# Optimization experiments

Measured on AMD Instinct MI355X. Metric: run time of the kernel, lower is better.

Reference implementation:

```python
import jax, jax.numpy as jnp
import numpy as np
import math

H = 8          # num_heads
HD = 64        # head_dim = hidden_dim // num_heads
LN_EPS = 1e-5


def setup_inputs() -> dict:
    key = jax.random.key(0)
    ks = jax.random.split(key, 16)
    B, N, L, D = 16, 1024, 7, 512
    s = 1.0 / math.sqrt(D)
    current_features = jax.random.normal(ks[0], (B, N, D), jnp.float32)
    lagged_features = jax.random.normal(ks[1], (B, N, L, D), jnp.float32)
    lag_weights = jnp.ones((L,), jnp.float32)
    Wq = jax.random.normal(ks[2], (D, D), jnp.float32) * s
    bq = jnp.zeros((D,), jnp.float32)
    Wk = jax.random.normal(ks[3], (D, D), jnp.float32) * s
    bk = jnp.zeros((D,), jnp.float32)
    Wv = jax.random.normal(ks[4], (D, D), jnp.float32) * s
    bv = jnp.zeros((D,), jnp.float32)
    Wo = jax.random.normal(ks[5], (D, D), jnp.float32) * s
    bo = jnp.zeros((D,), jnp.float32)
    adj = jax.random.uniform(ks[6], (N, N), jnp.float32)
    adj_prior = adj / (jnp.sum(adj, axis=-1, keepdims=True) + 1e-8)
    ln_g = jnp.ones((D,), jnp.float32)
    ln_b = jnp.zeros((D,), jnp.float32)
    return dict(current_features=current_features, lagged_features=lagged_features,
                lag_weights=lag_weights, Wq=Wq, bq=bq, Wk=Wk, bk=bk, Wv=Wv, bv=bv,
                Wo=Wo, bo=bo, adj_prior=adj_prior, ln_g=ln_g, ln_b=ln_b)


def _layer_norm(x, g, b):
    mu = jnp.mean(x, axis=-1, keepdims=True)
    var = jnp.mean(jnp.square(x - mu), axis=-1, keepdims=True)
    return (x - mu) * jax.lax.rsqrt(var + LN_EPS) * g + b


def reference(current_features, lagged_features, lag_weights, Wq, bq, Wk, bk,
              Wv, bv, Wo, bo, adj_prior, ln_g, ln_b):
    B, N, D = current_features.shape
    # lag-weighted aggregation of past states
    lag_w = jax.nn.softmax(lag_weights)
    lagged_agg = jnp.einsum('bnld,l->bnd', lagged_features, lag_w)
    # projections (torch Linear: x @ W.T + b)
    Q = current_features @ Wq.T + bq
    K = lagged_agg @ Wk.T + bk
    V = lagged_agg @ Wv.T + bv
    Q = Q.reshape(B, N, H, HD)
    K = K.reshape(B, N, H, HD)
    V = V.reshape(B, N, H, HD)
    scale = math.sqrt(HD)
    # scores [B, H, N, N] with additive adjacency bias
    scores = jnp.einsum('bnhd,bmhd->bhnm', Q, K) / scale
    scores = scores + adj_prior[None, None, :, :] * 0.5
    attn = jax.nn.softmax(scores, axis=-1)
    out = jnp.einsum('bhnm,bmhd->bnhd', attn, V).reshape(B, N, D)
    out = out @ Wo.T + bo
    return _layer_norm(current_features + out, ln_g, ln_b)
```

## Files before the change

kernel.cpp:

```cpp
#include <hip/hip_runtime.h>
#include <math.h>

#define B_  16
#define N_  1024
#define L_  7
#define D_  512
#define H_  8
#define HD_ 64
#define BN_ (B_ * N_)

typedef __attribute__((ext_vector_type(4))) float f32x4;
typedef __attribute__((ext_vector_type(8))) short bf16x8;

__device__ __forceinline__ unsigned short f2bf(float f) {
  unsigned int u = __float_as_uint(f);
  u += 0x7fffu + ((u >> 16) & 1u);
  return (unsigned short)(u >> 16);
}
__device__ __forceinline__ unsigned int pack2(float lo, float hi) {
  return (unsigned int)f2bf(lo) | ((unsigned int)f2bf(hi) << 16);
}
__device__ __forceinline__ void load_lds16(const unsigned short* g, unsigned short* s) {
  __builtin_amdgcn_global_load_lds(
      (const __attribute__((address_space(1))) void*)g,
      (__attribute__((address_space(3))) void*)s, 16, 0, 0);
}

__global__ __launch_bounds__(256)
void cast_bf16_kernel(const float* __restrict__ src, unsigned short* __restrict__ dst,
                      int n8) {
  const int i = blockIdx.x * 256 + threadIdx.x;
  if (i >= n8) return;
  const float4 a = ((const float4*)src)[2 * i];
  const float4 b = ((const float4*)src)[2 * i + 1];
  uint4 o;
  o.x = pack2(a.x, a.y); o.y = pack2(a.z, a.w);
  o.z = pack2(b.x, b.y); o.w = pack2(b.z, b.w);
  ((uint4*)dst)[i] = o;
}

__global__ __launch_bounds__(256)
void cast_w4_kernel(const float* __restrict__ w0, const float* __restrict__ w1,
                    const float* __restrict__ w2, const float* __restrict__ w3,
                    unsigned short* __restrict__ o0, unsigned short* __restrict__ o1,
                    unsigned short* __restrict__ o2, unsigned short* __restrict__ o3) {
  const int y = blockIdx.y;
  const float* src = (y == 0) ? w0 : (y == 1) ? w1 : (y == 2) ? w2 : w3;
  unsigned short* dst = (y == 0) ? o0 : (y == 1) ? o1 : (y == 2) ? o2 : o3;
  const int i = blockIdx.x * 256 + threadIdx.x;
  const float4 a = ((const float4*)src)[2 * i];
  const float4 b = ((const float4*)src)[2 * i + 1];
  uint4 o;
  o.x = pack2(a.x, a.y); o.y = pack2(a.z, a.w);
  o.z = pack2(b.x, b.y); o.w = pack2(b.z, b.w);
  ((uint4*)dst)[i] = o;
}

__global__ __launch_bounds__(256)
void lag_agg_bf16_kernel(const float* __restrict__ lf, const float* __restrict__ lw,
                         unsigned short* __restrict__ out) {
  const int i = blockIdx.x * 256 + threadIdx.x;
  float wv[L_];
  float m = -INFINITY;
#pragma unroll
  for (int l = 0; l < L_; ++l) { wv[l] = lw[l]; m = fmaxf(m, wv[l]); }
  float s = 0.f;
#pragma unroll
  for (int l = 0; l < L_; ++l) { wv[l] = __expf(wv[l] - m); s += wv[l]; }
  const float inv = 1.f / s;

  const int d8 = i & (D_ / 8 - 1);
  const int bn = i >> 6;
  const float* src = lf + (size_t)bn * (L_ * D_) + d8 * 8;
  float acc[8] = {};
#pragma unroll
  for (int l = 0; l < L_; ++l) {
    const float4 v0 = *(const float4*)(src + l * D_);
    const float4 v1 = *(const float4*)(src + l * D_ + 4);
    const float wl = wv[l] * inv;
    acc[0] += v0.x * wl; acc[1] += v0.y * wl; acc[2] += v0.z * wl; acc[3] += v0.w * wl;
    acc[4] += v1.x * wl; acc[5] += v1.y * wl; acc[6] += v1.z * wl; acc[7] += v1.w * wl;
  }
  uint4 o;
  o.x = pack2(acc[0], acc[1]); o.y = pack2(acc[2], acc[3]);
  o.z = pack2(acc[4], acc[5]); o.w = pack2(acc[6], acc[7]);
  ((uint4*)out)[i] = o;
}

struct GJob {
  const unsigned short* A;
  const unsigned short* W;
  const float* bias;
  void* C;
  int mode;
};

__global__ __launch_bounds__(256)
void gemm_dbuf_kernel(GJob j0, GJob j1, GJob j2) {
  const GJob j = (blockIdx.z == 0) ? j0 : (blockIdx.z == 1) ? j1 : j2;
  __shared__ unsigned short As[2 * 128 * 64];
  __shared__ unsigned short Bs[2 * 128 * 64];
  const int t = threadIdx.x;
  const int w = t >> 6, l = t & 63;
  const int wm = w >> 1, wn = w & 1;
  const int lc = l & 15, lg = l >> 4;
  const int m0 = blockIdx.y << 7, n0 = blockIdx.x << 7;
  const int srow = l >> 3, sc = l & 7;
  const unsigned short* A = j.A;
  const unsigned short* W = j.W;

  f32x4 acc[4][4];
#pragma unroll
  for (int i = 0; i < 4; ++i)
#pragma unroll
    for (int jj = 0; jj < 4; ++jj)
#pragma unroll
      for (int e = 0; e < 4; ++e) acc[i][jj][e] = 0.f;

#pragma unroll
  for (int i = 0; i < 4; ++i) {
    const int rb = (w << 5) + (i << 3);
    const int row = rb + srow;
    const int c = sc ^ (row & 7);
    load_lds16(A + (size_t)(m0 + row) * D_ + (c << 3), As + rb * 64);
    load_lds16(W + (size_t)(n0 + row) * D_ + (c << 3), Bs + rb * 64);
  }

  int cur = 0;
  for (int k0 = 0; k0 < D_; k0 += 64) {
    __syncthreads();
    if (k0 + 64 < D_) {
      unsigned short* An = As + ((cur ^ 1) << 13);
      unsigned short* Bn = Bs + ((cur ^ 1) << 13);
#pragma unroll
      for (int i = 0; i < 4; ++i) {
        const int rb = (w << 5) + (i << 3);
        const int row = rb + srow;
        const int c = sc ^ (row & 7);
        load_lds16(A + (size_t)(m0 + row) * D_ + k0 + 64 + (c << 3), An + rb * 64);
        load_lds16(W + (size_t)(n0 + row) * D_ + k0 + 64 + (c << 3), Bn + rb * 64);
      }
    }
    const unsigned short* Ac = As + (cur << 13);
    const unsigned short* Bc = Bs + (cur << 13);
#pragma unroll
    for (int kb = 0; kb < 2; ++kb) {
      bf16x8 af[4], bfr[4];
#pragma unroll
      for (int mi = 0; mi < 4; ++mi) {
        const int row = (wm << 6) + (mi << 4) + lc;
        const int pos = ((kb << 2) + lg) ^ (row & 7);
        af[mi] = *(const bf16x8*)(Ac + row * 64 + (pos << 3));
      }
#pragma unroll
      for (int ni = 0; ni < 4; ++ni) {
        const int row = (wn << 6) + (ni << 4) + lc;
        const int pos = ((kb << 2) + lg) ^ (row & 7);
        bfr[ni] = *(const bf16x8*)(Bc + row * 64 + (pos << 3));
      }
#pragma unroll
      for (int mi = 0; mi < 4; ++mi)
#pragma unroll
        for (int ni = 0; ni < 4; ++ni)
          acc[mi][ni] = __builtin_amdgcn_mfma_f32_16x16x32_bf16(
              af[mi], bfr[ni], acc[mi][ni], 0, 0, 0);
    }
    cur ^= 1;
  }

  const int mode = j.mode;
#pragma unroll
  for (int ni = 0; ni < 4; ++ni) {
    const int n = n0 + (wn << 6) + (ni << 4) + lc;
    const float bv = j.bias[n];
#pragma unroll
    for (int mi = 0; mi < 4; ++mi) {
      const int mb = m0 + (wm << 6) + (mi << 4) + (lg << 2);
      if (mode == 2) {
        float* O = (float*)j.C;
#pragma unroll
        for (int e = 0; e < 4; ++e)
          O[(size_t)(mb + e) * D_ + n] = acc[mi][ni][e] + bv;
      } else if (mode == 0) {
        unsigned short* O = (unsigned short*)j.C;
#pragma unroll
        for (int e = 0; e < 4; ++e)
          O[(size_t)(mb + e) * D_ + n] = f2bf(acc[mi][ni][e] + bv);
      } else {
        unsigned short* O = (unsigned short*)j.C;
        const int bb = mb >> 10, hh = n >> 6, d = n & 63;
        uint2 pk;
        pk.x = pack2(acc[mi][ni][0] + bv, acc[mi][ni][1] + bv);
        pk.y = pack2(acc[mi][ni][2] + bv, acc[mi][ni][3] + bv);
        *(uint2*)(O + ((size_t)((bb << 3) + hh) * HD_ + d) * N_ + (mb & 1023)) = pk;
      }
    }
  }
}

__global__ __launch_bounds__(256)
void attn_bf16_kernel(const unsigned short* __restrict__ Q,
                      const unsigned short* __restrict__ K,
                      const unsigned short* __restrict__ Vt,
                      const float* __restrict__ adj,
                      unsigned short* __restrict__ Out) {
  const int bh = blockIdx.y, b = bh >> 3, h = bh & 7;
  const int q0 = blockIdx.x << 6;
  const int t = threadIdx.x, w = t >> 6, l = t & 63;
  const int lc = l & 15, lg = l >> 4;
  __shared__ unsigned short Qs[64 * 64];
  __shared__ unsigned short Ks[2 * 64 * 64];
  __shared__ unsigned short Vs[2 * 64 * 64];
  const unsigned short* Qg = Q + (size_t)b * N_ * D_ + h * HD_;
  const unsigned short* Kg = K + (size_t)b * N_ * D_ + h * HD_;
  const unsigned short* Vg = Vt + (size_t)((b << 3) + h) * HD_ * N_;

#pragma unroll
  for (int i = 0; i < 2; ++i) {
    const int rb = (w << 4) + (i << 3);
    const int row = rb + (l >> 3);
    const int c = (l & 7) ^ (row & 7);
    load_lds16(Qg + (size_t)(q0 + row) * D_ + (c << 3), Qs + rb * 64);
    load_lds16(Kg + (size_t)row * D_ + (c << 3), Ks + rb * 64);
    load_lds16(Vg + (size_t)row * N_ + (c << 3), Vs + rb * 64);
  }
  __syncthreads();

  bf16x8 qf[2];
#pragma unroll
  for (int kb = 0; kb < 2; ++kb) {
    const int row = (w << 4) + lc;
    const int pos = ((kb << 2) + lg) ^ (row & 7);
    qf[kb] = *(const bf16x8*)(Qs + row * 64 + (pos << 3));
  }

  float m_r = -INFINITY, l_r = 0.f;
  f32x4 o[4];
#pragma unroll
  for (int di = 0; di < 4; ++di)
#pragma unroll
    for (int e = 0; e < 4; ++e) o[di][e] = 0.f;
  const int myq = q0 + (w << 4) + lc;
  unsigned short* Pw = Qs + (w << 10);

  int cur = 0;
  for (int kt = 0; kt < 16; ++kt) {
    if (kt) __syncthreads();
    const int kv0 = kt << 6;
    if (kt < 15) {
      unsigned short* Kn = Ks + ((cur ^ 1) << 12);
      unsigned short* Vn = Vs + ((cur ^ 1) << 12);
#pragma unroll
      for (int i = 0; i < 2; ++i) {
        const int rb = (w << 4) + (i << 3);
        const int row = rb + (l >> 3);
        const int c = (l & 7) ^ (row & 7);
        load_lds16(Kg + (size_t)(kv0 + 64 + row) * D_ + (c << 3), Kn + rb * 64);
        load_lds16(Vg + (size_t)row * N_ + kv0 + 64 + (c << 3), Vn + rb * 64);
      }
    }
    f32x4 aj[4];
#pragma unroll
    for (int ni = 0; ni < 4; ++ni)
      aj[ni] = *(const f32x4*)(adj + (size_t)myq * N_ + kv0 + (ni << 4) + (lg << 2));

    const unsigned short* Kc = Ks + (cur << 12);
    const unsigned short* Vc = Vs + (cur << 12);

    f32x4 st[4];
#pragma unroll
    for (int ni = 0; ni < 4; ++ni)
#pragma unroll
      for (int e = 0; e < 4; ++e) st[ni][e] = 0.f;
#pragma unroll
    for (int ni = 0; ni < 4; ++ni)
#pragma unroll
      for (int kb = 0; kb < 2; ++kb) {
        const int row = (ni << 4) + lc;
        const int pos = ((kb << 2) + lg) ^ (row & 7);
        const bf16x8 kf = *(const bf16x8*)(Kc + row * 64 + (pos << 3));
        st[ni] = __builtin_amdgcn_mfma_f32_16x16x32_bf16(kf, qf[kb], st[ni], 0, 0, 0);
      }

    float tmax = -INFINITY;
#pragma unroll
    for (int ni = 0; ni < 4; ++ni)
#pragma unroll
      for (int e = 0; e < 4; ++e) {
        const float v = st[ni][e] * 0.125f + 0.5f * aj[ni][e];
        st[ni][e] = v;
        tmax = fmaxf(tmax, v);
      }
    tmax = fmaxf(tmax, __shfl_xor(tmax, 16));
    tmax = fmaxf(tmax, __shfl_xor(tmax, 32));
    const float mnew = fmaxf(m_r, tmax);
    const float alpha = __expf(m_r - mnew);
    float ts = 0.f;
#pragma unroll
    for (int ni = 0; ni < 4; ++ni)
#pragma unroll
      for (int e = 0; e < 4; ++e) {
        const float p = __expf(st[ni][e] - mnew);
        st[ni][e] = p;
        ts += p;
      }
    ts += __shfl_xor(ts, 16);
    ts += __shfl_xor(ts, 32);
    l_r = l_r * alpha + ts;
    m_r = mnew;
#pragma unroll
    for (int di = 0; di < 4; ++di)
#pragma unroll
      for (int e = 0; e < 4; ++e) o[di][e] *= alpha;

#pragma unroll
    for (int ni = 0; ni < 4; ++ni) {
      uint2 pr;
      pr.x = pack2(st[ni][0], st[ni][1]);
      pr.y = pack2(st[ni][2], st[ni][3]);
      const int schunk = (2 * ni + (lg >> 1)) ^ (lc & 7);
      *(uint2*)(Pw + lc * 64 + (schunk << 3) + ((lg & 1) << 2)) = pr;
    }

#pragma unroll
    for (int kb = 0; kb < 2; ++kb) {
      const int rchunk = ((kb << 2) + lg) ^ (lc & 7);
      const bf16x8 pb = *(const bf16x8*)(Pw + lc * 64 + (rchunk << 3));
#pragma unroll
      for (int di = 0; di < 4; ++di) {
        const int row = (di << 4) + lc;
        const int pos = ((kb << 2) + lg) ^ (row & 7);
        const bf16x8 vf = *(const bf16x8*)(Vc + row * 64 + (pos << 3));
        o[di] = __builtin_amdgcn_mfma_f32_16x16x32_bf16(vf, pb, o[di], 0, 0, 0);
      }
    }
    cur ^= 1;
  }

  const float inv = 1.f / l_r;
  unsigned short* Ob = Out + (size_t)(b * N_ + q0 + (w << 4) + lc) * D_ + h * HD_;
#pragma unroll
  for (int di = 0; di < 4; ++di) {
    uint2 pk;
    pk.x = pack2(o[di][0] * inv, o[di][1] * inv);
    pk.y = pack2(o[di][2] * inv, o[di][3] * inv);
    *(uint2*)(Ob + (di << 4) + (lg << 2)) = pk;
  }
}

__global__ __launch_bounds__(256)
void ln_kernel(float* __restrict__ Y, const float* __restrict__ Xr,
               const float* __restrict__ g, const float* __restrict__ bta) {
  const int row  = (blockIdx.x << 2) + (threadIdx.x >> 6);
  const int lane = threadIdx.x & 63;
  float* yrow = Y + (size_t)row * D_;
  const float* xrow = Xr + (size_t)row * D_;
  const int c0 = lane << 3;

  const float4 y0 = *(const float4*)(yrow + c0);
  const float4 y1 = *(const float4*)(yrow + c0 + 4);
  const float4 r0 = *(const float4*)(xrow + c0);
  const float4 r1 = *(const float4*)(xrow + c0 + 4);
  float x[8] = {y0.x + r0.x, y0.y + r0.y, y0.z + r0.z, y0.w + r0.w,
                y1.x + r1.x, y1.y + r1.y, y1.z + r1.z, y1.w + r1.w};

  float sum = 0.f;
#pragma unroll
  for (int u = 0; u < 8; ++u) sum += x[u];
#pragma unroll
  for (int off = 32; off >= 1; off >>= 1) sum += __shfl_xor(sum, off);
  const float mu = sum * (1.f / D_);

  float vs = 0.f;
#pragma unroll
  for (int u = 0; u < 8; ++u) { const float d = x[u] - mu; vs += d * d; }
#pragma unroll
  for (int off = 32; off >= 1; off >>= 1) vs += __shfl_xor(vs, off);
  const float var = vs * (1.f / D_) + 1e-5f;
  float rinv = rsqrtf(var);
  rinv = rinv * (1.5f - 0.5f * var * rinv * rinv);

  const float4 g0 = *(const float4*)(g + c0);
  const float4 g1 = *(const float4*)(g + c0 + 4);
  const float4 b0 = *(const float4*)(bta + c0);
  const float4 b1 = *(const float4*)(bta + c0 + 4);
  float4 o0, o1;
  o0.x = (x[0] - mu) * rinv * g0.x + b0.x;
  o0.y = (x[1] - mu) * rinv * g0.y + b0.y;
  o0.z = (x[2] - mu) * rinv * g0.z + b0.z;
  o0.w = (x[3] - mu) * rinv * g0.w + b0.w;
  o1.x = (x[4] - mu) * rinv * g1.x + b1.x;
  o1.y = (x[5] - mu) * rinv * g1.y + b1.y;
  o1.z = (x[6] - mu) * rinv * g1.z + b1.z;
  o1.w = (x[7] - mu) * rinv * g1.w + b1.w;
  *(float4*)(yrow + c0) = o0;
  *(float4*)(yrow + c0 + 4) = o1;
}

extern "C" void kernel_launch(void* const* d_in, const int* in_sizes, int n_in,
                              void* d_out, int out_size, void* d_ws, size_t ws_size,
                              hipStream_t stream) {
  const float* cur = (const float*)d_in[0];
  const float* lf  = (const float*)d_in[1];
  const float* lw  = (const float*)d_in[2];
  const float* Wq  = (const float*)d_in[3];
  const float* bq  = (const float*)d_in[4];
  const float* Wk  = (const float*)d_in[5];
  const float* bk  = (const float*)d_in[6];
  const float* Wv  = (const float*)d_in[7];
  const float* bv  = (const float*)d_in[8];
  const float* Wo  = (const float*)d_in[9];
  const float* bo  = (const float*)d_in[10];
  const float* adj = (const float*)d_in[11];
  const float* lng = (const float*)d_in[12];
  const float* lnb = (const float*)d_in[13];
  float* out = (float*)d_out;

  const size_t NE = (size_t)BN_ * D_;
  unsigned short* wsb   = (unsigned short*)d_ws;
  unsigned short* curb  = wsb;
  unsigned short* laggb = wsb + NE;
  unsigned short* Qb    = wsb + 2 * NE;
  unsigned short* Kb    = wsb + 3 * NE;
  unsigned short* Vtb   = wsb + 4 * NE;
  unsigned short* attnb = wsb + 5 * NE;
  unsigned short* Wqb   = wsb + 6 * NE;
  unsigned short* Wkb   = Wqb + (size_t)D_ * D_;
  unsigned short* Wvb   = Wkb + (size_t)D_ * D_;
  unsigned short* Wob   = Wvb + (size_t)D_ * D_;

  cast_bf16_kernel<<<BN_ * D_ / 8 / 256, 256, 0, stream>>>(cur, curb, BN_ * D_ / 8);
  cast_w4_kernel<<<dim3(D_ * D_ / 8 / 256, 4), 256, 0, stream>>>(
      Wq, Wk, Wv, Wo, Wqb, Wkb, Wvb, Wob);
  lag_agg_bf16_kernel<<<BN_ * D_ / 8 / 256, 256, 0, stream>>>(lf, lw, laggb);

  GJob jq{curb,  Wqb, bq, (void*)Qb,  0};
  GJob jk{laggb, Wkb, bk, (void*)Kb,  0};
  GJob jv{laggb, Wvb, bv, (void*)Vtb, 1};
  gemm_dbuf_kernel<<<dim3(D_ / 128, BN_ / 128, 3), 256, 0, stream>>>(jq, jk, jv);

  attn_bf16_kernel<<<dim3(N_ / 64, B_ * H_), 256, 0, stream>>>(Qb, Kb, Vtb, adj, attnb);

  GJob jo{attnb, Wob, bo, (void*)out, 2};
  gemm_dbuf_kernel<<<dim3(D_ / 128, BN_ / 128, 1), 256, 0, stream>>>(jo, jo, jo);

  ln_kernel<<<BN_ / 4, 256, 0, stream>>>(out, cur, lng, lnb);
}
```

Measured before the change: 583.9 us.

## Fuse prep kernels, single-buffer GEMM/attention LDS, fold scales into exp2 softmax

Merges the lag aggregation, current-feature cast and a pre-scaled adjacency copy into one prep kernel. The softmax scale and log2e are folded into the Q projection epilogue and the adjacency bias, so attention uses exp2, and the rescale of the running output is skipped when the row max grows by no more than a threshold. Both the GEMM and attention kernels drop LDS double buffering in favour of single buffers with two barriers per step, and add s_setprio around MFMA blocks. This lowers LDS use, which may raise occupancy, but global loads are no longer overlapped with compute, and bf16 rounding of the pre-scaled Q changes precision slightly.

```diff
diff --git a/kernel.cpp b/kernel.cpp
--- a/kernel.cpp
+++ b/kernel.cpp
@@ -9,6 +9,10 @@
 #define HD_ 64
 #define BN_ (B_ * N_)
 
+#define LOG2E_ 1.44269504088896f
+#define QSCALE_ (0.125f * LOG2E_)
+#define ADJSCALE_ (0.5f * LOG2E_)
+
 typedef __attribute__((ext_vector_type(4))) float f32x4;
 typedef __attribute__((ext_vector_type(8))) short bf16x8;
 
@@ -25,18 +29,61 @@
       (const __attribute__((address_space(1))) void*)g,
       (__attribute__((address_space(3))) void*)s, 16, 0, 0);
 }
+#if __has_builtin(__builtin_amdgcn_exp2f)
+__device__ __forceinline__ float exp2_(float x) { return __builtin_amdgcn_exp2f(x); }
+#else
+__device__ __forceinline__ float exp2_(float x) { return exp2f(x); }
+#endif
 
 __global__ __launch_bounds__(256)
-void cast_bf16_kernel(const float* __restrict__ src, unsigned short* __restrict__ dst,
-                      int n8) {
-  const int i = blockIdx.x * 256 + threadIdx.x;
-  if (i >= n8) return;
-  const float4 a = ((const float4*)src)[2 * i];
-  const float4 b = ((const float4*)src)[2 * i + 1];
-  uint4 o;
-  o.x = pack2(a.x, a.y); o.y = pack2(a.z, a.w);
-  o.z = pack2(b.x, b.y); o.w = pack2(b.z, b.w);
-  ((uint4*)dst)[i] = o;
+void prep_kernel(const float* __restrict__ lf, const float* __restrict__ lw,
+                 const float* __restrict__ cur, const float* __restrict__ adj,
+                 unsigned short* __restrict__ laggb, unsigned short* __restrict__ curb,
+                 float* __restrict__ adjh) {
+  const int bid = blockIdx.x;
+  if (bid < 4096) {
+    const int i = bid * 256 + threadIdx.x;
+    float wv[L_];
+    float m = -INFINITY;
+#pragma unroll
+    for (int l = 0; l < L_; ++l) { wv[l] = lw[l]; m = fmaxf(m, wv[l]); }
+    float s = 0.f;
+#pragma unroll
+    for (int l = 0; l < L_; ++l) { wv[l] = __expf(wv[l] - m); s += wv[l]; }
+    const float inv = 1.f / s;
+    const int d8 = i & (D_ / 8 - 1);
+    const int bn = i >> 6;
+    const float* src = lf + (size_t)bn * (L_ * D_) + d8 * 8;
+    float acc[8] = {};
+#pragma unroll
+    for (int l = 0; l < L_; ++l) {
+      const float4 v0 = *(const float4*)(src + l * D_);
+      const float4 v1 = *(const float4*)(src + l * D_ + 4);
+      const float wl = wv[l] * inv;
+      acc[0] += v0.x * wl; acc[1] += v0.y * wl; acc[2] += v0.z * wl; acc[3] += v0.w * wl;
+      acc[4] += v1.x * wl; acc[5] += v1.y * wl; acc[6] += v1.z * wl; acc[7] += v1.w * wl;
+    }
+    uint4 o;
+    o.x = pack2(acc[0], acc[1]); o.y = pack2(acc[2], acc[3]);
+    o.z = pack2(acc[4], acc[5]); o.w = pack2(acc[6], acc[7]);
+    ((uint4*)laggb)[i] = o;
+  } else if (bid < 8192) {
+    const int i = (bid - 4096) * 256 + threadIdx.x;
+    const float4 a = ((const float4*)cur)[2 * i];
+    const float4 b = ((const float4*)cur)[2 * i + 1];
+    uint4 o;
+    o.x = pack2(a.x, a.y); o.y = pack2(a.z, a.w);
+    o.z = pack2(b.x, b.y); o.w = pack2(b.z, b.w);
+    ((uint4*)curb)[i] = o;
+  } else {
+    const int i = (bid - 8192) * 256 + threadIdx.x;
+    float4 a = ((const float4*)adj)[2 * i];
+    float4 b = ((const float4*)adj)[2 * i + 1];
+    a.x *= ADJSCALE_; a.y *= ADJSCALE_; a.z *= ADJSCALE_; a.w *= ADJSCALE_;
+    b.x *= ADJSCALE_; b.y *= ADJSCALE_; b.z *= ADJSCALE_; b.w *= ADJSCALE_;
+    ((float4*)adjh)[2 * i] = a;
+    ((float4*)adjh)[2 * i + 1] = b;
+  }
 }
 
 __global__ __launch_bounds__(256)
@@ -56,50 +103,20 @@
   ((uint4*)dst)[i] = o;
 }
 
-__global__ __launch_bounds__(256)
-void lag_agg_bf16_kernel(const float* __restrict__ lf, const float* __restrict__ lw,
-                         unsigned short* __restrict__ out) {
-  const int i = blockIdx.x * 256 + threadIdx.x;
-  float wv[L_];
-  float m = -INFINITY;
-#pragma unroll
-  for (int l = 0; l < L_; ++l) { wv[l] = lw[l]; m = fmaxf(m, wv[l]); }
-  float s = 0.f;
-#pragma unroll
-  for (int l = 0; l < L_; ++l) { wv[l] = __expf(wv[l] - m); s += wv[l]; }
-  const float inv = 1.f / s;
-
-  const int d8 = i & (D_ / 8 - 1);
-  const int bn = i >> 6;
-  const float* src = lf + (size_t)bn * (L_ * D_) + d8 * 8;
-  float acc[8] = {};
-#pragma unroll
-  for (int l = 0; l < L_; ++l) {
-    const float4 v0 = *(const float4*)(src + l * D_);
-    const float4 v1 = *(const float4*)(src + l * D_ + 4);
-    const float wl = wv[l] * inv;
-    acc[0] += v0.x * wl; acc[1] += v0.y * wl; acc[2] += v0.z * wl; acc[3] += v0.w * wl;
-    acc[4] += v1.x * wl; acc[5] += v1.y * wl; acc[6] += v1.z * wl; acc[7] += v1.w * wl;
-  }
-  uint4 o;
-  o.x = pack2(acc[0], acc[1]); o.y = pack2(acc[2], acc[3]);
-  o.z = pack2(acc[4], acc[5]); o.w = pack2(acc[6], acc[7]);
-  ((uint4*)out)[i] = o;
-}
-
 struct GJob {
   const unsigned short* A;
   const unsigned short* W;
   const float* bias;
   void* C;
   int mode;
+  float oscale;
 };
 
 __global__ __launch_bounds__(256)
-void gemm_dbuf_kernel(GJob j0, GJob j1, GJob j2) {
+void gemm_s_kernel(GJob j0, GJob j1, GJob j2) {
   const GJob j = (blockIdx.z == 0) ? j0 : (blockIdx.z == 1) ? j1 : j2;
-  __shared__ unsigned short As[2 * 128 * 64];
-  __shared__ unsigned short Bs[2 * 128 * 64];
+  __shared__ unsigned short As[128 * 64];
+  __shared__ unsigned short Bs[128 * 64];
   const int t = threadIdx.x;
   const int w = t >> 6, l = t & 63;
   const int wm = w >> 1, wn = w & 1;
@@ -117,32 +134,17 @@
 #pragma unroll
       for (int e = 0; e < 4; ++e) acc[i][jj][e] = 0.f;
 
-#pragma unroll
-  for (int i = 0; i < 4; ++i) {
-    const int rb = (w << 5) + (i << 3);
-    const int row = rb + srow;
-    const int c = sc ^ (row & 7);
-    load_lds16(A + (size_t)(m0 + row) * D_ + (c << 3), As + rb * 64);
-    load_lds16(W + (size_t)(n0 + row) * D_ + (c << 3), Bs + rb * 64);
-  }
-
-  int cur = 0;
   for (int k0 = 0; k0 < D_; k0 += 64) {
     __syncthreads();
-    if (k0 + 64 < D_) {
-      unsigned short* An = As + ((cur ^ 1) << 13);
-      unsigned short* Bn = Bs + ((cur ^ 1) << 13);
-#pragma unroll
-      for (int i = 0; i < 4; ++i) {
-        const int rb = (w << 5) + (i << 3);
-        const int row = rb + srow;
-        const int c = sc ^ (row & 7);
-        load_lds16(A + (size_t)(m0 + row) * D_ + k0 + 64 + (c << 3), An + rb * 64);
-        load_lds16(W + (size_t)(n0 + row) * D_ + k0 + 64 + (c << 3), Bn + rb * 64);
-      }
-    }
-    const unsigned short* Ac = As + (cur << 13);
-    const unsigned short* Bc = Bs + (cur << 13);
+#pragma unroll
+    for (int i = 0; i < 4; ++i) {
+      const int rb = (w << 5) + (i << 3);
+      const int row = rb + srow;
+      const int c = sc ^ (row & 7);
+      load_lds16(A + (size_t)(m0 + row) * D_ + k0 + (c << 3), As + rb * 64);
+      load_lds16(W + (size_t)(n0 + row) * D_ + k0 + (c << 3), Bs + rb * 64);
+    }
+    __syncthreads();
 #pragma unroll
     for (int kb = 0; kb < 2; ++kb) {
       bf16x8 af[4], bfr[4];
@@ -150,25 +152,27 @@
       for (int mi = 0; mi < 4; ++mi) {
         const int row = (wm << 6) + (mi << 4) + lc;
         const int pos = ((kb << 2) + lg) ^ (row & 7);
-        af[mi] = *(const bf16x8*)(Ac + row * 64 + (pos << 3));
+        af[mi] = *(const bf16x8*)(As + row * 64 + (pos << 3));
       }
 #pragma unroll
       for (int ni = 0; ni < 4; ++ni) {
         const int row = (wn << 6) + (ni << 4) + lc;
         const int pos = ((kb << 2) + lg) ^ (row & 7);
-        bfr[ni] = *(const bf16x8*)(Bc + row * 64 + (pos << 3));
-      }
+        bfr[ni] = *(const bf16x8*)(Bs + row * 64 + (pos << 3));
+      }
+      __builtin_amdgcn_s_setprio(1);
 #pragma unroll
       for (int mi = 0; mi < 4; ++mi)
 #pragma unroll
         for (int ni = 0; ni < 4; ++ni)
           acc[mi][ni] = __builtin_amdgcn_mfma_f32_16x16x32_bf16(
               af[mi], bfr[ni], acc[mi][ni], 0, 0, 0);
-    }
-    cur ^= 1;
+      __builtin_amdgcn_s_setprio(0);
+    }
   }
 
   const int mode = j.mode;
+  const float osc = j.oscale;
 #pragma unroll
   for (int ni = 0; ni < 4; ++ni) {
     const int n = n0 + (wn << 6) + (ni << 4) + lc;
@@ -185,7 +189,7 @@
         unsigned short* O = (unsigned short*)j.C;
 #pragma unroll
         for (int e = 0; e < 4; ++e)
-          O[(size_t)(mb + e) * D_ + n] = f2bf(acc[mi][ni][e] + bv);
+          O[(size_t)(mb + e) * D_ + n] = f2bf((acc[mi][ni][e] + bv) * osc);
       } else {
         unsigned short* O = (unsigned short*)j.C;
         const int bb = mb >> 10, hh = n >> 6, d = n & 63;
@@ -202,15 +206,15 @@
 void attn_bf16_kernel(const unsigned short* __restrict__ Q,
                       const unsigned short* __restrict__ K,
                       const unsigned short* __restrict__ Vt,
-                      const float* __restrict__ adj,
+                      const float* __restrict__ adjh,
                       unsigned short* __restrict__ Out) {
   const int bh = blockIdx.y, b = bh >> 3, h = bh & 7;
   const int q0 = blockIdx.x << 6;
   const int t = threadIdx.x, w = t >> 6, l = t & 63;
   const int lc = l & 15, lg = l >> 4;
   __shared__ unsigned short Qs[64 * 64];
-  __shared__ unsigned short Ks[2 * 64 * 64];
-  __shared__ unsigned short Vs[2 * 64 * 64];
+  __shared__ unsigned short Ks[64 * 64];
+  __shared__ unsigned short Vs[64 * 64];
   const unsigned short* Qg = Q + (size_t)b * N_ * D_ + h * HD_;
   const unsigned short* Kg = K + (size_t)b * N_ * D_ + h * HD_;
   const unsigned short* Vg = Vt + (size_t)((b << 3) + h) * HD_ * N_;
@@ -221,8 +225,6 @@
     const int row = rb + (l >> 3);
     const int c = (l & 7) ^ (row & 7);
     load_lds16(Qg + (size_t)(q0 + row) * D_ + (c << 3), Qs + rb * 64);
-    load_lds16(Kg + (size_t)row * D_ + (c << 3), Ks + rb * 64);
-    load_lds16(Vg + (size_t)row * N_ + (c << 3), Vs + rb * 64);
   }
   __syncthreads();
 
@@ -243,75 +245,73 @@
   const int myq = q0 + (w << 4) + lc;
   unsigned short* Pw = Qs + (w << 10);
 
-  int cur = 0;
   for (int kt = 0; kt < 16; ++kt) {
-    if (kt) __syncthreads();
     const int kv0 = kt << 6;
-    if (kt < 15) {
-      unsigned short* Kn = Ks + ((cur ^ 1) << 12);
-      unsigned short* Vn = Vs + ((cur ^ 1) << 12);
-#pragma unroll
-      for (int i = 0; i < 2; ++i) {
-        const int rb = (w << 4) + (i << 3);
-        const int row = rb + (l >> 3);
-        const int c = (l & 7) ^ (row & 7);
-        load_lds16(Kg + (size_t)(kv0 + 64 + row) * D_ + (c << 3), Kn + rb * 64);
-        load_lds16(Vg + (size_t)row * N_ + kv0 + 64 + (c << 3), Vn + rb * 64);
-      }
+    __syncthreads();
+#pragma unroll
+    for (int i = 0; i < 2; ++i) {
+      const int rb = (w << 4) + (i << 3);
+      const int row = rb + (l >> 3);
+      const int c = (l & 7) ^ (row & 7);
+      load_lds16(Kg + (size_t)(kv0 + row) * D_ + (c << 3), Ks + rb * 64);
+      load_lds16(Vg + (size_t)row * N_ + kv0 + (c << 3), Vs + rb * 64);
     }
     f32x4 aj[4];
 #pragma unroll
     for (int ni = 0; ni < 4; ++ni)
-      aj[ni] = *(const f32x4*)(adj + (size_t)myq * N_ + kv0 + (ni << 4) + (lg << 2));
-
-    const unsigned short* Kc = Ks + (cur << 12);
-    const unsigned short* Vc = Vs + (cur << 12);
+      aj[ni] = *(const f32x4*)(adjh + (size_t)myq * N_ + kv0 + (ni << 4) + (lg << 2));
+    __syncthreads();
 
     f32x4 st[4];
 #pragma unroll
     for (int ni = 0; ni < 4; ++ni)
 #pragma unroll
       for (int e = 0; e < 4; ++e) st[ni][e] = 0.f;
+    __builtin_amdgcn_s_setprio(1);
 #pragma unroll
     for (int ni = 0; ni < 4; ++ni)
 #pragma unroll
       for (int kb = 0; kb < 2; ++kb) {
         const int row = (ni << 4) + lc;
         const int pos = ((kb << 2) + lg) ^ (row & 7);
-        const bf16x8 kf = *(const bf16x8*)(Kc + row * 64 + (pos << 3));
+        const bf16x8 kf = *(const bf16x8*)(Ks + row * 64 + (pos << 3));
         st[ni] = __builtin_amdgcn_mfma_f32_16x16x32_bf16(kf, qf[kb], st[ni], 0, 0, 0);
       }
+    __builtin_amdgcn_s_setprio(0);
 
     float tmax = -INFINITY;
 #pragma unroll
     for (int ni = 0; ni < 4; ++ni)
 #pragma unroll
       for (int e = 0; e < 4; ++e) {
-        const float v = st[ni][e] * 0.125f + 0.5f * aj[ni][e];
+        const float v = st[ni][e] + aj[ni][e];
         st[ni][e] = v;
         tmax = fmaxf(tmax, v);
       }
     tmax = fmaxf(tmax, __shfl_xor(tmax, 16));
     tmax = fmaxf(tmax, __shfl_xor(tmax, 32));
-    const float mnew = fmaxf(m_r, tmax);
-    const float alpha = __expf(m_r - mnew);
+    if (!__all(tmax <= m_r + 8.f)) {
+      const float mnew = fmaxf(m_r, tmax);
+      const float alpha = exp2_(m_r - mnew);
+      l_r *= alpha;
+#pragma unroll
+      for (int di = 0; di < 4; ++di)
+#pragma unroll
+        for (int e = 0; e < 4; ++e) o[di][e] *= alpha;
+      m_r = mnew;
+    }
     float ts = 0.f;
 #pragma unroll
     for (int ni = 0; ni < 4; ++ni)
 #pragma unroll
       for (int e = 0; e < 4; ++e) {
-        const float p = __expf(st[ni][e] - mnew);
+        const float p = exp2_(st[ni][e] - m_r);
         st[ni][e] = p;
         ts += p;
       }
     ts += __shfl_xor(ts, 16);
     ts += __shfl_xor(ts, 32);
-    l_r = l_r * alpha + ts;
-    m_r = mnew;
-#pragma unroll
-    for (int di = 0; di < 4; ++di)
-#pragma unroll
-      for (int e = 0; e < 4; ++e) o[di][e] *= alpha;
+    l_r += ts;
 
 #pragma unroll
     for (int ni = 0; ni < 4; ++ni) {
@@ -326,15 +326,16 @@
     for (int kb = 0; kb < 2; ++kb) {
       const int rchunk = ((kb << 2) + lg) ^ (lc & 7);
       const bf16x8 pb = *(const bf16x8*)(Pw + lc * 64 + (rchunk << 3));
+      __builtin_amdgcn_s_setprio(1);
 #pragma unroll
       for (int di = 0; di < 4; ++di) {
         const int row = (di << 4) + lc;
         const int pos = ((kb << 2) + lg) ^ (row & 7);
-        const bf16x8 vf = *(const bf16x8*)(Vc + row * 64 + (pos << 3));
+        const bf16x8 vf = *(const bf16x8*)(Vs + row * 64 + (pos << 3));
         o[di] = __builtin_amdgcn_mfma_f32_16x16x32_bf16(vf, pb, o[di], 0, 0, 0);
       }
-    }
-    cur ^= 1;
+      __builtin_amdgcn_s_setprio(0);
+    }
   }
 
   const float inv = 1.f / l_r;
@@ -428,21 +429,21 @@
   unsigned short* Wkb   = Wqb + (size_t)D_ * D_;
   unsigned short* Wvb   = Wkb + (size_t)D_ * D_;
   unsigned short* Wob   = Wvb + (size_t)D_ * D_;
-
-  cast_bf16_kernel<<<BN_ * D_ / 8 / 256, 256, 0, stream>>>(cur, curb, BN_ * D_ / 8);
+  float*          adjh  = (float*)(Wob + (size_t)D_ * D_);
+
+  prep_kernel<<<8704, 256, 0, stream>>>(lf, lw, cur, adj, laggb, curb, adjh);
   cast_w4_kernel<<<dim3(D_ * D_ / 8 / 256, 4), 256, 0, stream>>>(
       Wq, Wk, Wv, Wo, Wqb, Wkb, Wvb, Wob);
-  lag_agg_bf16_kernel<<<BN_ * D_ / 8 / 256, 256, 0, stream>>>(lf, lw, laggb);
-
-  GJob jq{curb,  Wqb, bq, (void*)Qb,  0};
-  GJob jk{laggb, Wkb, bk, (void*)Kb,  0};
-  GJob jv{laggb, Wvb, bv, (void*)Vtb, 1};
-  gemm_dbuf_kernel<<<dim3(D_ / 128, BN_ / 128, 3), 256, 0, stream>>>(jq, jk, jv);
-
-  attn_bf16_kernel<<<dim3(N_ / 64, B_ * H_), 256, 0, stream>>>(Qb, Kb, Vtb, adj, attnb);
-
-  GJob jo{attnb, Wob, bo, (void*)out, 2};
-  gemm_dbuf_kernel<<<dim3(D_ / 128, BN_ / 128, 1), 256, 0, stream>>>(jo, jo, jo);
+
+  GJob jq{curb,  Wqb, bq, (void*)Qb,  0, QSCALE_};
+  GJob jk{laggb, Wkb, bk, (void*)Kb,  0, 1.0f};
+  GJob jv{laggb, Wvb, bv, (void*)Vtb, 1, 1.0f};
+  gemm_s_kernel<<<dim3(D_ / 128, BN_ / 128, 3), 256, 0, stream>>>(jq, jk, jv);
+
+  attn_bf16_kernel<<<dim3(N_ / 64, B_ * H_), 256, 0, stream>>>(Qb, Kb, Vtb, adjh, attnb);
+
+  GJob jo{attnb, Wob, bo, (void*)out, 2, 1.0f};
+  gemm_s_kernel<<<dim3(D_ / 128, BN_ / 128, 1), 256, 0, stream>>>(jo, jo, jo);
 
   ln_kernel<<<BN_ / 4, 256, 0, stream>>>(out, cur, lng, lnb);
 }
```

New measurement: 547.7 us. 6.2% less time.
